# Kernel tuning notes

Measured on AMD Instinct MI355X. Metric: run time of the kernel, lower is better.

The kernel has to match this reference:

```python
import jax, jax.numpy as jnp
import numpy as np

NN = 50000   # num nodes
NE = 10000   # num hyperedges
E = 300000   # num incidences
H = 256      # h_dim == input_dim


def _prelu(x, alpha):
    return jnp.where(x > 0, x, alpha * x)


def setup_inputs() -> dict:
    key = jax.random.key(0)
    ks = jax.random.split(key, 16)
    s = 1.0 / np.sqrt(H)
    inp = {
        "n_feat": jax.random.normal(ks[0], (NN, H), jnp.float32),
        "he_feat": jax.random.normal(ks[1], (NE, H), jnp.float32),
        "node_idx": jax.random.randint(ks[2], (E,), 0, NN),
        "hedge_idx": jax.random.randint(ks[3], (E,), 0, NE),
        # positive degree-style normalization tensors (offset avoids div-by-~0)
        "node_reg_weight": jax.random.uniform(ks[4], (NN,), jnp.float32) + 0.5,
        "node_reg_sum": jax.random.uniform(ks[5], (NN,), jnp.float32) + 0.5,
        "hedge_reg_weight": jax.random.uniform(ks[6], (NE,), jnp.float32) + 0.5,
        "hedge_reg_sum": jax.random.uniform(ks[7], (NE,), jnp.float32) + 0.5,
        # learned params
        "W_in": jax.random.uniform(ks[8], (H, H), jnp.float32, -s, s),
        "b_in": jax.random.uniform(ks[9], (H,), jnp.float32, -s, s),
        "W_n2e": jax.random.uniform(ks[10], (H, H), jnp.float32, -s, s),
        "b_n2e": jax.random.uniform(ks[11], (H,), jnp.float32, -s, s),
        "W_e2n": jax.random.uniform(ks[12], (H, H), jnp.float32, -s, s),
        "b_e2n": jax.random.uniform(ks[13], (H,), jnp.float32, -s, s),
        "alpha": jnp.asarray(0.25, jnp.float32),  # PReLU (single shared param)
    }
    return inp


def reference(n_feat, he_feat, node_idx, hedge_idx,
              node_reg_weight, node_reg_sum, hedge_reg_weight, hedge_reg_sum,
              W_in, b_in, W_n2e, b_n2e, W_e2n, b_e2n, alpha):
    # input2hidden
    nfeat = n_feat @ W_in.T + b_in                       # [NN, H]

    # --- node -> hedge ('in' edges: src=node, dst=hedge) ---
    Wh_n = nfeat @ W_n2e.T + b_n2e                       # [NN, H]
    w_in = node_reg_weight[node_idx] / hedge_reg_sum[hedge_idx]   # [E]
    msg = w_in[:, None] * Wh_n[node_idx]                 # [E, H] gather-multiply
    h_hedge = jax.ops.segment_sum(msg, hedge_idx, num_segments=NE)
    efeat = _prelu(h_hedge, alpha)                       # [NE, H]

    # --- hedge -> node ('con' edges: src=hedge, dst=node) ---
    Wh_e = efeat @ W_e2n.T + b_e2n                       # [NE, H]
    w_con = hedge_reg_weight[hedge_idx] / node_reg_sum[node_idx]  # [E]
    msg2 = w_con[:, None] * Wh_e[hedge_idx]              # [E, H]
    h_node = jax.ops.segment_sum(msg2, node_idx, num_segments=NN)
    nfeat_out = _prelu(h_node, alpha)                    # [NN, H]

    return nfeat_out, efeat
```

## Files before the change

kernel.cpp:

```cpp
#include <hip/hip_runtime.h>

#define NNODE  50000
#define NHEDGE 10000
#define NEDGE  300000
#define HD     256
#define NS     (NHEDGE + NNODE)
#define CVT32_B (((NNODE*HD)/32 + 255) / 256)
#define PAD    32
#define CAP_H  128
#define CAP_N  48

typedef __attribute__((ext_vector_type(8))) short bf16x8;
typedef __attribute__((ext_vector_type(8))) unsigned short u16x8;
typedef __attribute__((ext_vector_type(4))) float f32x4;

__device__ __forceinline__ float prelu(float v, float a){ return v > 0.f ? v : a*v; }
__device__ __forceinline__ unsigned short f2bf(float f){
  unsigned u = __float_as_uint(f);
  return (unsigned short)((u + 0x7FFFu + ((u>>16)&1u)) >> 16);
}
__device__ __forceinline__ float bf2f(unsigned short h){
  return __uint_as_float(((unsigned)h) << 16);
}
__device__ __forceinline__ unsigned f2fp8(float x){
  unsigned u = __float_as_uint(x * 0x1p-120f);
  unsigned s = (u >> 24) & 0x80u;
  unsigned m = u & 0x7fffffffu;
  unsigned r = m + 0x7ffffu + ((m >> 20) & 1u);
  unsigned v = r >> 20;
  if(v > 0x7eu) v = 0x7eu;
  return v | s;
}
__device__ __forceinline__ float fp82f(unsigned b){
  unsigned mag = (b & 0x7fu) << 20;
  float f = __uint_as_float(mag) * 0x1p120f;
  return __uint_as_float(__float_as_uint(f) | ((b & 0x80u) << 24));
}

__global__ __launch_bounds__(256) void k_prep0(
    const float* __restrict__ W_in, const float* __restrict__ b_in,
    const float* __restrict__ W_n2e, const float* __restrict__ b_n2e,
    const float* __restrict__ W_e2n, const float* __restrict__ n_feat,
    const float* __restrict__ nrw,
    unsigned short* __restrict__ Wb0, unsigned short* __restrict__ Wb1,
    float* __restrict__ bc, int* __restrict__ cnts,
    unsigned char* __restrict__ tab8){
  int blk = blockIdx.x, t = threadIdx.x;
  if(blk < HD){
    int o = blk;
    int zi = o*256 + t;
    if(zi < NS) cnts[(size_t)zi*PAD] = 0;
    __shared__ float wn[HD];
    __shared__ float red[4];
    wn[t] = W_n2e[(size_t)o*HD + t];
    __syncthreads();
    float pb = wn[t] * b_in[t];
    #pragma unroll
    for(int d = 32; d > 0; d >>= 1) pb += __shfl_down(pb, d);
    if((t & 63) == 0) red[t >> 6] = pb;
    float acc = 0.f;
    #pragma unroll 8
    for(int h = 0; h < HD; ++h) acc += wn[h] * W_in[(size_t)h*HD + t];
    Wb0[(size_t)o*HD + t] = f2bf(acc);
    Wb1[(size_t)o*HD + t] = f2bf(W_e2n[(size_t)o*HD + t]);
    __syncthreads();
    if(t == 0) bc[o] = red[0] + red[1] + red[2] + red[3] + b_n2e[o];
  } else {
    int t32 = (blk - HD)*256 + t;
    if(t32 >= (NNODE*HD)/32) return;
    size_t f = (size_t)t32 * 32;
    float w = nrw[f >> 8];
    const float4* f4 = (const float4*)(n_feat + f);
    unsigned q[8];
    #pragma unroll
    for(int g = 0; g < 8; ++g){
      float4 a = f4[g];
      q[g] =  f2fp8(w*a.x)        | (f2fp8(w*a.y) << 8)
           | (f2fp8(w*a.z) << 16) | (f2fp8(w*a.w) << 24);
    }
    uint4* out = (uint4*)(tab8 + f);
    out[0] = make_uint4(q[0], q[1], q[2], q[3]);
    out[1] = make_uint4(q[4], q[5], q[6], q[7]);
  }
}

__global__ void k_histfill(const int* __restrict__ node_idx, const int* __restrict__ hedge_idx,
                           const float* __restrict__ nrw, int* __restrict__ cnts,
                           int2* __restrict__ bkt_h, int* __restrict__ bkt_n){
  int e = blockIdx.x*256 + threadIdx.x;
  if(e < NEDGE){
    int j = hedge_idx[e];
    int n = node_idx[e];
    int p = atomicAdd(&cnts[(size_t)j*PAD], 1);
    if(p < CAP_H) bkt_h[(size_t)j*CAP_H + p] = make_int2(n, __float_as_int(nrw[n]));
    int q = atomicAdd(&cnts[(size_t)(NHEDGE + n)*PAD], 1);
    if(q < CAP_N) bkt_n[(size_t)n*CAP_N + q] = j;
  }
}

__global__ __launch_bounds__(256) void k_agg1(const unsigned char* __restrict__ tab8,
        const int2* __restrict__ bkt_h, const int* __restrict__ cnts,
        unsigned short* __restrict__ aggx_b, float* __restrict__ aggw){
  __shared__ float lacc[8][32][9];
  __shared__ float lsw[8];
  int tid = threadIdx.x;
  int half = tid >> 5;
  int sl   = tid & 31;
  int lane = tid & 63;
  int hb   = lane & 32;
  int j = blockIdx.x*2 + (half >> 2);
  int c = half & 3;
  int cnt = cnts[(size_t)j*PAD]; if(cnt > CAP_H) cnt = CAP_H;
  int Lc = (cnt + 3) >> 2;
  int lo = c*Lc; if(lo > cnt) lo = cnt;
  int hi = lo + Lc; if(hi > cnt) hi = cnt;
  int Len = hi - lo;
  const int2* bh = bkt_h + (size_t)j*CAP_H + lo;
  int2 meta = (sl < Len) ? bh[sl] : make_int2(0, 0);
  const uint2* tab = (const uint2*)tab8;
  float acc[8] = {0.f,0.f,0.f,0.f,0.f,0.f,0.f,0.f};
  float sw = 0.f;
  uint2 v[16];
  #pragma unroll
  for(int k = 0; k < 16; ++k){
    if(k < Len){
      int src = __shfl(meta.x, hb + k);
      sw += __int_as_float(__shfl(meta.y, hb + k));
      v[k] = tab[(size_t)src*32 + sl];
    }
  }
  #pragma unroll
  for(int k = 0; k < 16; ++k){
    if(k < Len){
      uint2 cv = v[k];
      acc[0] += fp82f(cv.x);       acc[1] += fp82f(cv.x >> 8);
      acc[2] += fp82f(cv.x >> 16); acc[3] += fp82f(cv.x >> 24);
      acc[4] += fp82f(cv.y);       acc[5] += fp82f(cv.y >> 8);
      acc[6] += fp82f(cv.y >> 16); acc[7] += fp82f(cv.y >> 24);
    }
  }
  for(int k = 16; k < Len; ++k){
    int2 mk = bh[k];
    sw += __int_as_float(mk.y);
    uint2 cv = tab[(size_t)mk.x*32 + sl];
    acc[0] += fp82f(cv.x);       acc[1] += fp82f(cv.x >> 8);
    acc[2] += fp82f(cv.x >> 16); acc[3] += fp82f(cv.x >> 24);
    acc[4] += fp82f(cv.y);       acc[5] += fp82f(cv.y >> 8);
    acc[6] += fp82f(cv.y >> 16); acc[7] += fp82f(cv.y >> 24);
  }
  #pragma unroll
  for(int cc = 0; cc < 8; ++cc) lacc[half][sl][cc] = acc[cc];
  if(sl == 0) lsw[half] = sw;
  __syncthreads();
  if((half & 3) == 0){
    u16x8 ob;
    #pragma unroll
    for(int cc = 0; cc < 8; ++cc){
      float s = lacc[half][sl][cc] + lacc[half+1][sl][cc]
              + lacc[half+2][sl][cc] + lacc[half+3][sl][cc];
      ob[cc] = f2bf(s);
    }
    ((u16x8*)aggx_b)[(size_t)j*32 + sl] = ob;
    if(sl == 0) aggw[j] = lsw[half] + lsw[half+1] + lsw[half+2] + lsw[half+3];
  }
}

__global__ __launch_bounds__(256) void k_gemm01(
    const unsigned short* __restrict__ xb, const unsigned short* __restrict__ Wb0,
    const unsigned short* __restrict__ Wb1,
    const float* __restrict__ aggw, const float* __restrict__ hrs,
    const float* __restrict__ hrw, const float* __restrict__ bc,
    const float* __restrict__ be, const float* __restrict__ alpha_p,
    float* __restrict__ out_ef, unsigned short* __restrict__ ef_b,
    unsigned short* __restrict__ y_b){
  int wv = threadIdx.x >> 6, lane = threadIdx.x & 63;
  int m0 = blockIdx.x*32;
  int n0 = wv*64;
  int lr = lane & 15, lk = (lane >> 4) << 3, rb = (lane >> 4) << 2;
  float alpha = *alpha_p;
  const bf16x8 zero8 = {0,0,0,0,0,0,0,0};
  {
    f32x4 acc[2][4];
    #pragma unroll
    for(int a = 0; a < 2; ++a)
      #pragma unroll
      for(int b = 0; b < 4; ++b) acc[a][b] = (f32x4){0.f,0.f,0.f,0.f};
    #pragma unroll
    for(int kc = 0; kc < HD; kc += 32){
      bf16x8 af[2], bfr[4];
      #pragma unroll
      for(int mi = 0; mi < 2; ++mi){
        int r = m0 + mi*16 + lr;
        af[mi] = (r < NHEDGE) ? *(const bf16x8*)&xb[(size_t)r*HD + kc + lk] : zero8;
      }
      #pragma unroll
      for(int ni = 0; ni < 4; ++ni){
        int c = n0 + ni*16 + lr;
        bfr[ni] = *(const bf16x8*)&Wb0[(size_t)c*HD + kc + lk];
      }
      #pragma unroll
      for(int mi = 0; mi < 2; ++mi)
        #pragma unroll
        for(int ni = 0; ni < 4; ++ni)
          acc[mi][ni] = __builtin_amdgcn_mfma_f32_16x16x32_bf16(af[mi], bfr[ni], acc[mi][ni], 0, 0, 0);
    }
    #pragma unroll
    for(int mi = 0; mi < 2; ++mi){
      #pragma unroll
      for(int jj = 0; jj < 4; ++jj){
        int r = m0 + mi*16 + rb + jj;
        if(r < NHEDGE){
          float ra = aggw[r];
          float inv = 1.f / hrs[r];
          #pragma unroll
          for(int ni = 0; ni < 4; ++ni){
            int c = n0 + ni*16 + lr;
            float v = (acc[mi][ni][jj] + ra*bc[c]) * inv;
            v = prelu(v, alpha);
            out_ef[(size_t)r*HD + c] = v;
            ef_b[(size_t)r*HD + c] = f2bf(v);
          }
        }
      }
    }
  }
  __syncthreads();
  {
    f32x4 acc[2][4];
    #pragma unroll
    for(int a = 0; a < 2; ++a)
      #pragma unroll
      for(int b = 0; b < 4; ++b) acc[a][b] = (f32x4){0.f,0.f,0.f,0.f};
    #pragma unroll
    for(int kc = 0; kc < HD; kc += 32){
      bf16x8 af[2], bfr[4];
      #pragma unroll
      for(int mi = 0; mi < 2; ++mi){
        int r = m0 + mi*16 + lr;
        af[mi] = (r < NHEDGE) ? *(const bf16x8*)&ef_b[(size_t)r*HD + kc + lk] : zero8;
      }
      #pragma unroll
      for(int ni = 0; ni < 4; ++ni){
        int c = n0 + ni*16 + lr;
        bfr[ni] = *(const bf16x8*)&Wb1[(size_t)c*HD + kc + lk];
      }
      #pragma unroll
      for(int mi = 0; mi < 2; ++mi)
        #pragma unroll
        for(int ni = 0; ni < 4; ++ni)
          acc[mi][ni] = __builtin_amdgcn_mfma_f32_16x16x32_bf16(af[mi], bfr[ni], acc[mi][ni], 0, 0, 0);
    }
    #pragma unroll
    for(int mi = 0; mi < 2; ++mi){
      #pragma unroll
      for(int jj = 0; jj < 4; ++jj){
        int r = m0 + mi*16 + rb + jj;
        if(r < NHEDGE){
          float ra = hrw[r];
          #pragma unroll
          for(int ni = 0; ni < 4; ++ni){
            int c = n0 + ni*16 + lr;
            float v = ra * (acc[mi][ni][jj] + be[c]);
            y_b[(size_t)r*HD + c] = f2bf(v);
          }
        }
      }
    }
  }
}

__global__ __launch_bounds__(256) void k_agg2(const unsigned short* __restrict__ yb,
        const int* __restrict__ bkt_n, const int* __restrict__ cnts,
        const float* __restrict__ nrs, const float* __restrict__ alpha_p,
        float* __restrict__ out_nodes){
  int tid = threadIdx.x;
  int half = tid >> 5;
  int sl   = tid & 31;
  int lane = tid & 63;
  int hb   = lane & 32;
  int i = blockIdx.x*8 + half;
  int cnt = cnts[(size_t)(NHEDGE + i)*PAD]; if(cnt > CAP_N) cnt = CAP_N;
  const int* bn = bkt_n + (size_t)i*CAP_N;
  int meta = (sl < cnt) ? bn[sl] : 0;
  const u16x8* tab = (const u16x8*)yb;
  float acc[8] = {0.f,0.f,0.f,0.f,0.f,0.f,0.f,0.f};
  u16x8 v[12];
  #pragma unroll
  for(int k = 0; k < 12; ++k){
    if(k < cnt){
      int j = __shfl(meta, hb + k);
      v[k] = tab[(size_t)j*32 + sl];
    }
  }
  #pragma unroll
  for(int k = 0; k < 12; ++k){
    if(k < cnt){
      #pragma unroll
      for(int c = 0; c < 8; ++c) acc[c] += bf2f(v[k][c]);
    }
  }
  for(int k = 12; k < cnt; ++k){
    int j = bn[k];
    u16x8 cv = tab[(size_t)j*32 + sl];
    #pragma unroll
    for(int c = 0; c < 8; ++c) acc[c] += bf2f(cv[c]);
  }
  float inv = 1.f / nrs[i];
  float a = *alpha_p;
  float4 o1, o2;
  o1.x = prelu(acc[0]*inv, a); o1.y = prelu(acc[1]*inv, a);
  o1.z = prelu(acc[2]*inv, a); o1.w = prelu(acc[3]*inv, a);
  o2.x = prelu(acc[4]*inv, a); o2.y = prelu(acc[5]*inv, a);
  o2.z = prelu(acc[6]*inv, a); o2.w = prelu(acc[7]*inv, a);
  *(float4*)&out_nodes[(size_t)i*HD + sl*8]     = o1;
  *(float4*)&out_nodes[(size_t)i*HD + sl*8 + 4] = o2;
}

extern "C" void kernel_launch(void* const* d_in, const int* in_sizes, int n_in,
                              void* d_out, int out_size, void* d_ws, size_t ws_size,
                              hipStream_t stream){
  const float* n_feat   = (const float*)d_in[0];
  const int*   node_idx  = (const int*)d_in[2];
  const int*   hedge_idx = (const int*)d_in[3];
  const float* nrw  = (const float*)d_in[4];
  const float* nrs  = (const float*)d_in[5];
  const float* hrw  = (const float*)d_in[6];
  const float* hrs  = (const float*)d_in[7];
  const float* W_in  = (const float*)d_in[8];
  const float* b_in  = (const float*)d_in[9];
  const float* W_n2e = (const float*)d_in[10];
  const float* b_n2e = (const float*)d_in[11];
  const float* W_e2n = (const float*)d_in[12];
  const float* b_e2n = (const float*)d_in[13];
  const float* alpha = (const float*)d_in[14];

  float* out_nodes = (float*)d_out;
  float* out_efeat = out_nodes + (size_t)NNODE * HD;

  unsigned char* tab8 = (unsigned char*)out_nodes;

  char* p = (char*)d_ws;
  auto take = [&](size_t bytes) -> void* {
    void* r = (void*)p;
    p += (bytes + 255) & ~(size_t)255;
    return r;
  };
  unsigned short* Wb0     = (unsigned short*)take((size_t)HD*HD*2);
  unsigned short* Wb1     = (unsigned short*)take((size_t)HD*HD*2);
  float*          bc      = (float*)take(HD*4);
  float*          aggw    = (float*)take(NHEDGE*4);
  unsigned short* aggx_b  = (unsigned short*)take((size_t)NHEDGE*HD*2);
  unsigned short* efeat_b = (unsigned short*)take((size_t)NHEDGE*HD*2);
  int*            cnts    = (int*)take((size_t)NS*PAD*4);
  int2*           bkt_h   = (int2*)take((size_t)NHEDGE*CAP_H*8);
  int*            bkt_n   = (int*)take((size_t)NNODE*CAP_N*4);
  unsigned short* ybuf_b  = aggx_b;

  k_prep0<<<HD + CVT32_B, 256, 0, stream>>>(W_in, b_in, W_n2e, b_n2e, W_e2n,
                                            n_feat, nrw, Wb0, Wb1, bc, cnts, tab8);
  k_histfill<<<(NEDGE+255)/256, 256, 0, stream>>>(node_idx, hedge_idx, nrw,
                                                  cnts, bkt_h, bkt_n);
  k_agg1<<<NHEDGE/2, 256, 0, stream>>>(tab8, bkt_h, cnts, aggx_b, aggw);
  k_gemm01<<<(NHEDGE + 31)/32, 256, 0, stream>>>(aggx_b, Wb0, Wb1, aggw, hrs, hrw,
                                                 bc, b_e2n, alpha,
                                                 out_efeat, efeat_b, ybuf_b);
  k_agg2<<<NNODE/8, 256, 0, stream>>>(ybuf_b, bkt_n, cnts, nrs, alpha, out_nodes);
}
```

Before: 143.6 us.

## Reorder hedge-to-node stage to aggregate fp8 efeat before the W_e2n GEMM

The hedge-to-node step now gathers a compact fp8 copy of efeat, weighted per edge by hrw, into per-node bf16 sums. A new node-sized GEMM then applies W_e2n, the bias scaled by the summed weights, 1/nrs and PReLU. Before, the code ran the GEMM on hedges first and gathered bf16 rows. The aim is to shrink the gathered table so the random gathers stay in cache. In exchange, the GEMM runs over 50000 node rows instead of 10000 hedge rows, and a 25 MB bf16 intermediate is written and read back. Separately, the node feature table for the first aggregation changes from fp8 to bf16, which doubles the bytes gathered there but improves accuracy.

```diff
diff --git a/kernel.cpp b/kernel.cpp
--- a/kernel.cpp
+++ b/kernel.cpp
@@ -44,7 +44,7 @@
     const float* __restrict__ nrw,
     unsigned short* __restrict__ Wb0, unsigned short* __restrict__ Wb1,
     float* __restrict__ bc, int* __restrict__ cnts,
-    unsigned char* __restrict__ tab8){
+    unsigned short* __restrict__ tabw){
   int blk = blockIdx.x, t = threadIdx.x;
   if(blk < HD){
     int o = blk;
@@ -71,22 +71,26 @@
     size_t f = (size_t)t32 * 32;
     float w = nrw[f >> 8];
     const float4* f4 = (const float4*)(n_feat + f);
-    unsigned q[8];
-    #pragma unroll
-    for(int g = 0; g < 8; ++g){
-      float4 a = f4[g];
-      q[g] =  f2fp8(w*a.x)        | (f2fp8(w*a.y) << 8)
-           | (f2fp8(w*a.z) << 16) | (f2fp8(w*a.w) << 24);
-    }
-    uint4* out = (uint4*)(tab8 + f);
-    out[0] = make_uint4(q[0], q[1], q[2], q[3]);
-    out[1] = make_uint4(q[4], q[5], q[6], q[7]);
+    float4 a0 = f4[0], a1 = f4[1], a2 = f4[2], a3 = f4[3];
+    float4 a4 = f4[4], a5 = f4[5], a6 = f4[6], a7 = f4[7];
+    u16x8* out = (u16x8*)(tabw + f);
+    u16x8 o0, o1, o2, o3;
+    o0[0]=f2bf(w*a0.x); o0[1]=f2bf(w*a0.y); o0[2]=f2bf(w*a0.z); o0[3]=f2bf(w*a0.w);
+    o0[4]=f2bf(w*a1.x); o0[5]=f2bf(w*a1.y); o0[6]=f2bf(w*a1.z); o0[7]=f2bf(w*a1.w);
+    o1[0]=f2bf(w*a2.x); o1[1]=f2bf(w*a2.y); o1[2]=f2bf(w*a2.z); o1[3]=f2bf(w*a2.w);
+    o1[4]=f2bf(w*a3.x); o1[5]=f2bf(w*a3.y); o1[6]=f2bf(w*a3.z); o1[7]=f2bf(w*a3.w);
+    o2[0]=f2bf(w*a4.x); o2[1]=f2bf(w*a4.y); o2[2]=f2bf(w*a4.z); o2[3]=f2bf(w*a4.w);
+    o2[4]=f2bf(w*a5.x); o2[5]=f2bf(w*a5.y); o2[6]=f2bf(w*a5.z); o2[7]=f2bf(w*a5.w);
+    o3[0]=f2bf(w*a6.x); o3[1]=f2bf(w*a6.y); o3[2]=f2bf(w*a6.z); o3[3]=f2bf(w*a6.w);
+    o3[4]=f2bf(w*a7.x); o3[5]=f2bf(w*a7.y); o3[6]=f2bf(w*a7.z); o3[7]=f2bf(w*a7.w);
+    out[0] = o0; out[1] = o1; out[2] = o2; out[3] = o3;
   }
 }
 
 __global__ void k_histfill(const int* __restrict__ node_idx, const int* __restrict__ hedge_idx,
-                           const float* __restrict__ nrw, int* __restrict__ cnts,
-                           int2* __restrict__ bkt_h, int* __restrict__ bkt_n){
+                           const float* __restrict__ nrw, const float* __restrict__ hrw,
+                           int* __restrict__ cnts,
+                           int2* __restrict__ bkt_h, int2* __restrict__ bkt_n){
   int e = blockIdx.x*256 + threadIdx.x;
   if(e < NEDGE){
     int j = hedge_idx[e];
@@ -94,11 +98,11 @@
     int p = atomicAdd(&cnts[(size_t)j*PAD], 1);
     if(p < CAP_H) bkt_h[(size_t)j*CAP_H + p] = make_int2(n, __float_as_int(nrw[n]));
     int q = atomicAdd(&cnts[(size_t)(NHEDGE + n)*PAD], 1);
-    if(q < CAP_N) bkt_n[(size_t)n*CAP_N + q] = j;
-  }
-}
-
-__global__ __launch_bounds__(256) void k_agg1(const unsigned char* __restrict__ tab8,
+    if(q < CAP_N) bkt_n[(size_t)n*CAP_N + q] = make_int2(j, __float_as_int(hrw[j]));
+  }
+}
+
+__global__ __launch_bounds__(256) void k_agg1(const unsigned short* __restrict__ tabw,
         const int2* __restrict__ bkt_h, const int* __restrict__ cnts,
         unsigned short* __restrict__ aggx_b, float* __restrict__ aggw){
   __shared__ float lacc[8][32][9];
@@ -117,10 +121,10 @@
   int Len = hi - lo;
   const int2* bh = bkt_h + (size_t)j*CAP_H + lo;
   int2 meta = (sl < Len) ? bh[sl] : make_int2(0, 0);
-  const uint2* tab = (const uint2*)tab8;
+  const u16x8* tab = (const u16x8*)tabw;
   float acc[8] = {0.f,0.f,0.f,0.f,0.f,0.f,0.f,0.f};
   float sw = 0.f;
-  uint2 v[16];
+  u16x8 v[16];
   #pragma unroll
   for(int k = 0; k < 16; ++k){
     if(k < Len){
@@ -132,21 +136,16 @@
   #pragma unroll
   for(int k = 0; k < 16; ++k){
     if(k < Len){
-      uint2 cv = v[k];
-      acc[0] += fp82f(cv.x);       acc[1] += fp82f(cv.x >> 8);
-      acc[2] += fp82f(cv.x >> 16); acc[3] += fp82f(cv.x >> 24);
-      acc[4] += fp82f(cv.y);       acc[5] += fp82f(cv.y >> 8);
-      acc[6] += fp82f(cv.y >> 16); acc[7] += fp82f(cv.y >> 24);
+      #pragma unroll
+      for(int cc = 0; cc < 8; ++cc) acc[cc] += bf2f(v[k][cc]);
     }
   }
   for(int k = 16; k < Len; ++k){
     int2 mk = bh[k];
     sw += __int_as_float(mk.y);
-    uint2 cv = tab[(size_t)mk.x*32 + sl];
-    acc[0] += fp82f(cv.x);       acc[1] += fp82f(cv.x >> 8);
-    acc[2] += fp82f(cv.x >> 16); acc[3] += fp82f(cv.x >> 24);
-    acc[4] += fp82f(cv.y);       acc[5] += fp82f(cv.y >> 8);
-    acc[6] += fp82f(cv.y >> 16); acc[7] += fp82f(cv.y >> 24);
+    u16x8 cv = tab[(size_t)mk.x*32 + sl];
+    #pragma unroll
+    for(int cc = 0; cc < 8; ++cc) acc[cc] += bf2f(cv[cc]);
   }
   #pragma unroll
   for(int cc = 0; cc < 8; ++cc) lacc[half][sl][cc] = acc[cc];
@@ -165,114 +164,65 @@
   }
 }
 
-__global__ __launch_bounds__(256) void k_gemm01(
+__global__ __launch_bounds__(256) void k_gemm0(
     const unsigned short* __restrict__ xb, const unsigned short* __restrict__ Wb0,
-    const unsigned short* __restrict__ Wb1,
     const float* __restrict__ aggw, const float* __restrict__ hrs,
-    const float* __restrict__ hrw, const float* __restrict__ bc,
-    const float* __restrict__ be, const float* __restrict__ alpha_p,
-    float* __restrict__ out_ef, unsigned short* __restrict__ ef_b,
-    unsigned short* __restrict__ y_b){
+    const float* __restrict__ bc, const float* __restrict__ alpha_p,
+    float* __restrict__ out_ef, unsigned char* __restrict__ ef8){
   int wv = threadIdx.x >> 6, lane = threadIdx.x & 63;
   int m0 = blockIdx.x*32;
   int n0 = wv*64;
   int lr = lane & 15, lk = (lane >> 4) << 3, rb = (lane >> 4) << 2;
   float alpha = *alpha_p;
   const bf16x8 zero8 = {0,0,0,0,0,0,0,0};
-  {
-    f32x4 acc[2][4];
-    #pragma unroll
-    for(int a = 0; a < 2; ++a)
+  f32x4 acc[2][4];
+  #pragma unroll
+  for(int a = 0; a < 2; ++a)
+    #pragma unroll
+    for(int b = 0; b < 4; ++b) acc[a][b] = (f32x4){0.f,0.f,0.f,0.f};
+  #pragma unroll
+  for(int kc = 0; kc < HD; kc += 32){
+    bf16x8 af[2], bfr[4];
+    #pragma unroll
+    for(int mi = 0; mi < 2; ++mi){
+      int r = m0 + mi*16 + lr;
+      af[mi] = (r < NHEDGE) ? *(const bf16x8*)&xb[(size_t)r*HD + kc + lk] : zero8;
+    }
+    #pragma unroll
+    for(int ni = 0; ni < 4; ++ni){
+      int c = n0 + ni*16 + lr;
+      bfr[ni] = *(const bf16x8*)&Wb0[(size_t)c*HD + kc + lk];
+    }
+    #pragma unroll
+    for(int mi = 0; mi < 2; ++mi)
       #pragma unroll
-      for(int b = 0; b < 4; ++b) acc[a][b] = (f32x4){0.f,0.f,0.f,0.f};
-    #pragma unroll
-    for(int kc = 0; kc < HD; kc += 32){
-      bf16x8 af[2], bfr[4];
-      #pragma unroll
-      for(int mi = 0; mi < 2; ++mi){
-        int r = m0 + mi*16 + lr;
-        af[mi] = (r < NHEDGE) ? *(const bf16x8*)&xb[(size_t)r*HD + kc + lk] : zero8;
-      }
-      #pragma unroll
-      for(int ni = 0; ni < 4; ++ni){
-        int c = n0 + ni*16 + lr;
-        bfr[ni] = *(const bf16x8*)&Wb0[(size_t)c*HD + kc + lk];
-      }
-      #pragma unroll
-      for(int mi = 0; mi < 2; ++mi)
+      for(int ni = 0; ni < 4; ++ni)
+        acc[mi][ni] = __builtin_amdgcn_mfma_f32_16x16x32_bf16(af[mi], bfr[ni], acc[mi][ni], 0, 0, 0);
+  }
+  #pragma unroll
+  for(int mi = 0; mi < 2; ++mi){
+    #pragma unroll
+    for(int jj = 0; jj < 4; ++jj){
+      int r = m0 + mi*16 + rb + jj;
+      if(r < NHEDGE){
+        float ra = aggw[r];
+        float inv = 1.f / hrs[r];
         #pragma unroll
-        for(int ni = 0; ni < 4; ++ni)
-          acc[mi][ni] = __builtin_amdgcn_mfma_f32_16x16x32_bf16(af[mi], bfr[ni], acc[mi][ni], 0, 0, 0);
-    }
-    #pragma unroll
-    for(int mi = 0; mi < 2; ++mi){
-      #pragma unroll
-      for(int jj = 0; jj < 4; ++jj){
-        int r = m0 + mi*16 + rb + jj;
-        if(r < NHEDGE){
-          float ra = aggw[r];
-          float inv = 1.f / hrs[r];
-          #pragma unroll
-          for(int ni = 0; ni < 4; ++ni){
-            int c = n0 + ni*16 + lr;
-            float v = (acc[mi][ni][jj] + ra*bc[c]) * inv;
-            v = prelu(v, alpha);
-            out_ef[(size_t)r*HD + c] = v;
-            ef_b[(size_t)r*HD + c] = f2bf(v);
-          }
+        for(int ni = 0; ni < 4; ++ni){
+          int c = n0 + ni*16 + lr;
+          float v = (acc[mi][ni][jj] + ra*bc[c]) * inv;
+          v = prelu(v, alpha);
+          out_ef[(size_t)r*HD + c] = v;
+          ef8[(size_t)r*HD + c] = (unsigned char)f2fp8(v);
         }
       }
     }
   }
-  __syncthreads();
-  {
-    f32x4 acc[2][4];
-    #pragma unroll
-    for(int a = 0; a < 2; ++a)
-      #pragma unroll
-      for(int b = 0; b < 4; ++b) acc[a][b] = (f32x4){0.f,0.f,0.f,0.f};
-    #pragma unroll
-    for(int kc = 0; kc < HD; kc += 32){
-      bf16x8 af[2], bfr[4];
-      #pragma unroll
-      for(int mi = 0; mi < 2; ++mi){
-        int r = m0 + mi*16 + lr;
-        af[mi] = (r < NHEDGE) ? *(const bf16x8*)&ef_b[(size_t)r*HD + kc + lk] : zero8;
-      }
-      #pragma unroll
-      for(int ni = 0; ni < 4; ++ni){
-        int c = n0 + ni*16 + lr;
-        bfr[ni] = *(const bf16x8*)&Wb1[(size_t)c*HD + kc + lk];
-      }
-      #pragma unroll
-      for(int mi = 0; mi < 2; ++mi)
-        #pragma unroll
-        for(int ni = 0; ni < 4; ++ni)
-          acc[mi][ni] = __builtin_amdgcn_mfma_f32_16x16x32_bf16(af[mi], bfr[ni], acc[mi][ni], 0, 0, 0);
-    }
-    #pragma unroll
-    for(int mi = 0; mi < 2; ++mi){
-      #pragma unroll
-      for(int jj = 0; jj < 4; ++jj){
-        int r = m0 + mi*16 + rb + jj;
-        if(r < NHEDGE){
-          float ra = hrw[r];
-          #pragma unroll
-          for(int ni = 0; ni < 4; ++ni){
-            int c = n0 + ni*16 + lr;
-            float v = ra * (acc[mi][ni][jj] + be[c]);
-            y_b[(size_t)r*HD + c] = f2bf(v);
-          }
-        }
-      }
-    }
-  }
-}
-
-__global__ __launch_bounds__(256) void k_agg2(const unsigned short* __restrict__ yb,
-        const int* __restrict__ bkt_n, const int* __restrict__ cnts,
-        const float* __restrict__ nrs, const float* __restrict__ alpha_p,
-        float* __restrict__ out_nodes){
+}
+
+__global__ __launch_bounds__(256) void k_agg2p(const unsigned char* __restrict__ ef8,
+        const int2* __restrict__ bkt_n, const int* __restrict__ cnts,
+        unsigned short* __restrict__ h_pre, float* __restrict__ sw_n){
   int tid = threadIdx.x;
   int half = tid >> 5;
   int sl   = tid & 31;
@@ -280,40 +230,101 @@
   int hb   = lane & 32;
   int i = blockIdx.x*8 + half;
   int cnt = cnts[(size_t)(NHEDGE + i)*PAD]; if(cnt > CAP_N) cnt = CAP_N;
-  const int* bn = bkt_n + (size_t)i*CAP_N;
-  int meta = (sl < cnt) ? bn[sl] : 0;
-  const u16x8* tab = (const u16x8*)yb;
+  const int2* bn = bkt_n + (size_t)i*CAP_N;
+  int2 meta = (sl < cnt) ? bn[sl] : make_int2(0, 0);
+  const uint2* tab = (const uint2*)ef8;
   float acc[8] = {0.f,0.f,0.f,0.f,0.f,0.f,0.f,0.f};
-  u16x8 v[12];
+  float sw = 0.f;
+  uint2 v[12];
+  float wv[12];
   #pragma unroll
   for(int k = 0; k < 12; ++k){
     if(k < cnt){
-      int j = __shfl(meta, hb + k);
+      int j = __shfl(meta.x, hb + k);
+      wv[k] = __int_as_float(__shfl(meta.y, hb + k));
+      sw += wv[k];
       v[k] = tab[(size_t)j*32 + sl];
     }
   }
   #pragma unroll
   for(int k = 0; k < 12; ++k){
     if(k < cnt){
+      uint2 cv = v[k]; float w = wv[k];
+      acc[0] += w*fp82f(cv.x);       acc[1] += w*fp82f(cv.x >> 8);
+      acc[2] += w*fp82f(cv.x >> 16); acc[3] += w*fp82f(cv.x >> 24);
+      acc[4] += w*fp82f(cv.y);       acc[5] += w*fp82f(cv.y >> 8);
+      acc[6] += w*fp82f(cv.y >> 16); acc[7] += w*fp82f(cv.y >> 24);
+    }
+  }
+  for(int k = 12; k < cnt; ++k){
+    int2 mk = bn[k];
+    float w = __int_as_float(mk.y);
+    sw += w;
+    uint2 cv = tab[(size_t)mk.x*32 + sl];
+    acc[0] += w*fp82f(cv.x);       acc[1] += w*fp82f(cv.x >> 8);
+    acc[2] += w*fp82f(cv.x >> 16); acc[3] += w*fp82f(cv.x >> 24);
+    acc[4] += w*fp82f(cv.y);       acc[5] += w*fp82f(cv.y >> 8);
+    acc[6] += w*fp82f(cv.y >> 16); acc[7] += w*fp82f(cv.y >> 24);
+  }
+  u16x8 ob;
+  #pragma unroll
+  for(int c = 0; c < 8; ++c) ob[c] = f2bf(acc[c]);
+  ((u16x8*)h_pre)[(size_t)i*32 + sl] = ob;
+  if(sl == 0) sw_n[i] = sw;
+}
+
+__global__ __launch_bounds__(256) void k_gemm2(
+    const unsigned short* __restrict__ xb, const unsigned short* __restrict__ Wb1,
+    const float* __restrict__ sw_n, const float* __restrict__ nrs,
+    const float* __restrict__ be, const float* __restrict__ alpha_p,
+    float* __restrict__ out_nodes){
+  int wv = threadIdx.x >> 6, lane = threadIdx.x & 63;
+  int m0 = blockIdx.x*32;
+  int n0 = wv*64;
+  int lr = lane & 15, lk = (lane >> 4) << 3, rb = (lane >> 4) << 2;
+  float alpha = *alpha_p;
+  const bf16x8 zero8 = {0,0,0,0,0,0,0,0};
+  f32x4 acc[2][4];
+  #pragma unroll
+  for(int a = 0; a < 2; ++a)
+    #pragma unroll
+    for(int b = 0; b < 4; ++b) acc[a][b] = (f32x4){0.f,0.f,0.f,0.f};
+  #pragma unroll
+  for(int kc = 0; kc < HD; kc += 32){
+    bf16x8 af[2], bfr[4];
+    #pragma unroll
+    for(int mi = 0; mi < 2; ++mi){
+      int r = m0 + mi*16 + lr;
+      af[mi] = (r < NNODE) ? *(const bf16x8*)&xb[(size_t)r*HD + kc + lk] : zero8;
+    }
+    #pragma unroll
+    for(int ni = 0; ni < 4; ++ni){
+      int c = n0 + ni*16 + lr;
+      bfr[ni] = *(const bf16x8*)&Wb1[(size_t)c*HD + kc + lk];
+    }
+    #pragma unroll
+    for(int mi = 0; mi < 2; ++mi)
       #pragma unroll
-      for(int c = 0; c < 8; ++c) acc[c] += bf2f(v[k][c]);
-    }
-  }
-  for(int k = 12; k < cnt; ++k){
-    int j = bn[k];
-    u16x8 cv = tab[(size_t)j*32 + sl];
-    #pragma unroll
-    for(int c = 0; c < 8; ++c) acc[c] += bf2f(cv[c]);
-  }
-  float inv = 1.f / nrs[i];
-  float a = *alpha_p;
-  float4 o1, o2;
-  o1.x = prelu(acc[0]*inv, a); o1.y = prelu(acc[1]*inv, a);
-  o1.z = prelu(acc[2]*inv, a); o1.w = prelu(acc[3]*inv, a);
-  o2.x = prelu(acc[4]*inv, a); o2.y = prelu(acc[5]*inv, a);
-  o2.z = prelu(acc[6]*inv, a); o2.w = prelu(acc[7]*inv, a);
-  *(float4*)&out_nodes[(size_t)i*HD + sl*8]     = o1;
-  *(float4*)&out_nodes[(size_t)i*HD + sl*8 + 4] = o2;
+      for(int ni = 0; ni < 4; ++ni)
+        acc[mi][ni] = __builtin_amdgcn_mfma_f32_16x16x32_bf16(af[mi], bfr[ni], acc[mi][ni], 0, 0, 0);
+  }
+  #pragma unroll
+  for(int mi = 0; mi < 2; ++mi){
+    #pragma unroll
+    for(int jj = 0; jj < 4; ++jj){
+      int r = m0 + mi*16 + rb + jj;
+      if(r < NNODE){
+        float sw = sw_n[r];
+        float inv = 1.f / nrs[r];
+        #pragma unroll
+        for(int ni = 0; ni < 4; ++ni){
+          int c = n0 + ni*16 + lr;
+          float v = (acc[mi][ni][jj] + sw*be[c]) * inv;
+          out_nodes[(size_t)r*HD + c] = prelu(v, alpha);
+        }
+      }
+    }
+  }
 }
 
 extern "C" void kernel_launch(void* const* d_in, const int* in_sizes, int n_in,
@@ -337,7 +348,7 @@
   float* out_nodes = (float*)d_out;
   float* out_efeat = out_nodes + (size_t)NNODE * HD;
 
-  unsigned char* tab8 = (unsigned char*)out_nodes;
+  unsigned short* tabw = (unsigned short*)out_nodes;
 
   char* p = (char*)d_ws;
   auto take = [&](size_t bytes) -> void* {
@@ -349,20 +360,22 @@
   unsigned short* Wb1     = (unsigned short*)take((size_t)HD*HD*2);
   float*          bc      = (float*)take(HD*4);
   float*          aggw    = (float*)take(NHEDGE*4);
+  float*          sw_n    = (float*)take(NNODE*4);
   unsigned short* aggx_b  = (unsigned short*)take((size_t)NHEDGE*HD*2);
-  unsigned short* efeat_b = (unsigned short*)take((size_t)NHEDGE*HD*2);
+  unsigned char*  ef8     = (unsigned char*)take((size_t)NHEDGE*HD);
+  unsigned short* h_pre   = (unsigned short*)take((size_t)NNODE*HD*2);
   int*            cnts    = (int*)take((size_t)NS*PAD*4);
   int2*           bkt_h   = (int2*)take((size_t)NHEDGE*CAP_H*8);
-  int*            bkt_n   = (int*)take((size_t)NNODE*CAP_N*4);
-  unsigned short* ybuf_b  = aggx_b;
+  int2*           bkt_n   = (int2*)take((size_t)NNODE*CAP_N*8);
 
   k_prep0<<<HD + CVT32_B, 256, 0, stream>>>(W_in, b_in, W_n2e, b_n2e, W_e2n,
-                                            n_feat, nrw, Wb0, Wb1, bc, cnts, tab8);
-  k_histfill<<<(NEDGE+255)/256, 256, 0, stream>>>(node_idx, hedge_idx, nrw,
+                                            n_feat, nrw, Wb0, Wb1, bc, cnts, tabw);
+  k_histfill<<<(NEDGE+255)/256, 256, 0, stream>>>(node_idx, hedge_idx, nrw, hrw,
                                                   cnts, bkt_h, bkt_n);
-  k_agg1<<<NHEDGE/2, 256, 0, stream>>>(tab8, bkt_h, cnts, aggx_b, aggw);
-  k_gemm01<<<(NHEDGE + 31)/32, 256, 0, stream>>>(aggx_b, Wb0, Wb1, aggw, hrs, hrw,
-                                                 bc, b_e2n, alpha,
-                                                 out_efeat, efeat_b, ybuf_b);
-  k_agg2<<<NNODE/8, 256, 0, stream>>>(ybuf_b, bkt_n, cnts, nrs, alpha, out_nodes);
-}
+  k_agg1<<<NHEDGE/2, 256, 0, stream>>>(tabw, bkt_h, cnts, aggx_b, aggw);
+  k_gemm0<<<(NHEDGE + 31)/32, 256, 0, stream>>>(aggx_b, Wb0, aggw, hrs, bc, alpha,
+                                                out_efeat, ef8);
+  k_agg2p<<<NNODE/8, 256, 0, stream>>>(ef8, bkt_n, cnts, h_pre, sw_n);
+  k_gemm2<<<(NNODE + 31)/32, 256, 0, stream>>>(h_pre, Wb1, sw_n, nrs, b_e2n, alpha,
+                                               out_nodes);
+}
```

Measured after the change: 185.8 us. 1.29x slower.
